# Optimization experiments

Hardware: AMD Instinct MI355X
Metric: run time of the kernel (lower is better)

## Reference

```python
import jax, jax.numpy as jnp
import numpy as np

N_KERNELS = 5
MUL_FACTOR = 2.0


def setup_inputs() -> dict:
    key = jax.random.key(0)
    k1, k2 = jax.random.split(key)
    x = jax.random.normal(k1, (8192, 64), dtype=jnp.float32)
    y = jax.random.normal(k2, (8192, 64), dtype=jnp.float32)
    return {"x": x, "y": y}


def reference(x, y):
    # bandwidth multipliers: mul_factor ** (arange(n) - n//2) -> [0.25,0.5,1,2,4]
    mults = MUL_FACTOR ** (jnp.arange(N_KERNELS, dtype=jnp.float32) - N_KERNELS // 2)

    z = jnp.concatenate([x, y], axis=0)  # [N, d], N = n + m
    n = x.shape[0]
    N = z.shape[0]

    # squared pairwise L2 distances: ||a||^2 + ||b||^2 - 2 a.b, clamped at 0
    sq = jnp.sum(z * z, axis=-1)  # [N]
    d2 = jnp.maximum(sq[:, None] + sq[None, :] - 2.0 * (z @ z.T), 0.0)  # [N, N]

    # data-dependent bandwidth: sum(d2) / (N^2 - N)
    bw = jnp.sum(d2) / (N * N - N)

    # multi-bandwidth RBF kernel, summed over kernels: [N, N]
    K = jnp.sum(jnp.exp(-d2[None, :, :] / (bw * mults)[:, None, None]), axis=0)

    XX = jnp.mean(K[:n, :n])
    XY = jnp.mean(K[:n, n:])
    YY = jnp.mean(K[n:, n:])
    return XX - 2.0 * XY + YY
```

## Files before the change

kernel.cpp:

```cpp
#include <hip/hip_runtime.h>
#include <hip/hip_bf16.h>

#define D 64

typedef __attribute__((ext_vector_type(8))) _Float16 half8;
typedef __attribute__((ext_vector_type(4))) float floatx4;

__global__ __launch_bounds__(256) void k_pre(const float* __restrict__ x, const float* __restrict__ y,
                                             int nx, _Float16* __restrict__ zh,
                                             float* __restrict__ sq, double* __restrict__ Tpart,
                                             float* __restrict__ Spart) {
    int tid = threadIdx.x;
    int lane = tid & 63, wid = tid >> 6;
    int t = blockIdx.x * 256 + tid;
    size_t e = (size_t)t * 8;
    int row = (int)(e >> 6);
    const float* src = (row < nx) ? (x + e) : (y + (e - (size_t)nx * D));
    float4 v0 = ((const float4*)src)[0];
    float4 v1 = ((const float4*)src)[1];
    half8 h;
    h[0]=(_Float16)v0.x; h[1]=(_Float16)v0.y; h[2]=(_Float16)v0.z; h[3]=(_Float16)v0.w;
    h[4]=(_Float16)v1.x; h[5]=(_Float16)v1.y; h[6]=(_Float16)v1.z; h[7]=(_Float16)v1.w;
    *(half8*)(zh + e) = h;
    float p = v0.x*v0.x + v0.y*v0.y + v0.z*v0.z + v0.w*v0.w
            + v1.x*v1.x + v1.y*v1.y + v1.z*v1.z + v1.w*v1.w;
    float s = p;
    s += __shfl_xor(s, 1);
    s += __shfl_xor(s, 2);
    s += __shfl_xor(s, 4);
    if ((tid & 7) == 0) sq[row] = s;

    __shared__ float colbuf[32][64];
    int rib = tid >> 3, cg = tid & 7;
    *(float4*)&colbuf[rib][cg * 8]     = v0;
    *(float4*)&colbuf[rib][cg * 8 + 4] = v1;

    double dp = (double)p;
    dp += __shfl_xor(dp, 1);
    dp += __shfl_xor(dp, 2);
    dp += __shfl_xor(dp, 4);
    dp += __shfl_xor(dp, 8);
    dp += __shfl_xor(dp, 16);
    dp += __shfl_xor(dp, 32);
    __shared__ double redw[4];
    if (lane == 0) redw[wid] = dp;
    __syncthreads();
    if (tid == 0) Tpart[blockIdx.x] = (redw[0] + redw[1]) + (redw[2] + redw[3]);

    if (tid < 64) {
        float cs = 0.f;
#pragma unroll
        for (int r2 = 0; r2 < 32; ++r2) cs += colbuf[r2][tid];
        Spart[blockIdx.x * 64 + tid] = cs;
    }
}

__global__ __launch_bounds__(256) void k_bw(const double* __restrict__ Tpart, int ntp,
                                            const float* __restrict__ Spart, int nsp,
                                            int N, float* __restrict__ cq_p) {
    int t = threadIdx.x;
    double Tp = 0.0;
    for (int b = t; b < ntp; b += 256) Tp += Tpart[b];

    int q = t >> 6, col = t & 63;
    int bpq = nsp >> 2;
    const float* sp = Spart + (size_t)(q * bpq) * 64 + col;
    float c0 = 0.f, c1 = 0.f, c2 = 0.f, c3 = 0.f;
    for (int b = 0; b < bpq; b += 4) {
        c0 += sp[(b + 0) * 64];
        c1 += sp[(b + 1) * 64];
        c2 += sp[(b + 2) * 64];
        c3 += sp[(b + 3) * 64];
    }
    __shared__ float cred[256];
    cred[t] = (c0 + c1) + (c2 + c3);

    __shared__ double red[256];
    red[t] = Tp;
    __syncthreads();
    for (int off = 128; off > 0; off >>= 1) {
        if (t < off) red[t] += red[t + off];
        __syncthreads();
    }
    double T = red[0];
    __shared__ double red2[64];
    if (t < 64) {
        float Sk = cred[t] + cred[t + 64] + cred[t + 128] + cred[t + 192];
        red2[t] = (double)Sk * (double)Sk;
    }
    __syncthreads();
    if (t == 0) {
        double S2 = 0.0;
        for (int i = 0; i < 64; ++i) S2 += red2[i];
        double sumd2 = 2.0 * (double)N * T - 2.0 * S2;
        double bw = sumd2 / ((double)N * (double)N - (double)N);
        cq_p[0] = (float)(1.4426950408889634 / (4.0 * bw));
    }
}

__global__ __launch_bounds__(256, 4) void k_mmd(const _Float16* __restrict__ zh,
                                                const float* __restrict__ sq,
                                                const float* __restrict__ cq_p,
                                                int nb, double* __restrict__ partial) {
    int bid = (nb - 1) - (int)blockIdx.x;
    int g = (int)((sqrtf(1.0f + 2.0f * (float)bid) - 1.0f) * 0.5f);
    while (2 * (g + 1) * (g + 2) <= bid) ++g;
    while (2 * g * (g + 1) > bid) --g;
    int r = bid - 2 * g * (g + 1);
    int gp1 = g + 1;
    int rig = r / gp1;
    int jc  = r - rig * gp1;
    int ib  = 4 * g + rig;

    int jstart = jc * 512;
    int jend   = (ib + 1) * 128;
    if (jend > jstart + 512) jend = jstart + 512;
    int njt = (jend - jstart) >> 4;
    int diag_j = ib * 128;

    int lane = threadIdx.x & 63;
    int wid  = threadIdx.x >> 6;
    int i0 = ib * 128 + wid * 32;

    float cq  = cq_p[0];
    float c2q = 2.0f * cq;

    int lrow = lane & 15;
    int kb = (lane >> 4) * 8;

    const _Float16* ar0 = zh + (size_t)(i0 + lrow) * D + kb;
    half8 a00 = *(const half8*)(ar0);
    half8 a01 = *(const half8*)(ar0 + 32);
    half8 a10 = *(const half8*)(ar0 + 16 * D);
    half8 a11 = *(const half8*)(ar0 + 16 * D + 32);

    int irh = (lane >> 4) * 4;
    float nai0[4], nai1[4];
#pragma unroll
    for (int rr = 0; rr < 4; ++rr) {
        nai0[rr] = -sq[i0 + irh + rr] * cq;
        nai1[rr] = -sq[i0 + 16 + irh + rr] * cq;
    }

    const _Float16* bptr = zh + (size_t)(jstart + lrow) * D + kb;
    const float* sqjp = sq + jstart + lrow;

    float acc = 0.f;

    auto compute = [&](half8 b0, half8 b1, float sqj, float wf) {
        float nbj = -sqj * cq;
        floatx4 d0 = {0.f, 0.f, 0.f, 0.f};
        floatx4 d1 = {0.f, 0.f, 0.f, 0.f};
        d0 = __builtin_amdgcn_mfma_f32_16x16x32_f16(a00, b0, d0, 0, 0, 0);
        d0 = __builtin_amdgcn_mfma_f32_16x16x32_f16(a01, b1, d0, 0, 0, 0);
        d1 = __builtin_amdgcn_mfma_f32_16x16x32_f16(a10, b0, d1, 0, 0, 0);
        d1 = __builtin_amdgcn_mfma_f32_16x16x32_f16(a11, b1, d1, 0, 0, 0);
        float part = 0.f;
#pragma unroll
        for (int rr = 0; rr < 4; ++rr) {
            float u0 = fminf(fmaf(d0[rr], c2q, nai0[rr] + nbj), 0.f);
            float u1 = fminf(fmaf(d1[rr], c2q, nai1[rr] + nbj), 0.f);
            float q0 = __builtin_amdgcn_exp2f(u0);
            float q1 = __builtin_amdgcn_exp2f(u1);
            float m01 = q0 * q0,   m11 = q1 * q1;
            float m02 = m01 * m01, m12 = m11 * m11;
            float m03 = m02 * m02, m13 = m12 * m12;
            float s0 = (q0 + m01) + (m02 + m03);
            float s1 = (q1 + m11) + (m12 + m13);
            part += fmaf(m03, m03, s0) + fmaf(m13, m13, s1);
        }
        acc = fmaf(part, wf, acc);
    };

    half8 b0A = *(const half8*)(bptr);
    half8 b1A = *(const half8*)(bptr + 32);
    float sA  = sqjp[0];
    half8 b0B = *(const half8*)(bptr + 16 * D);
    half8 b1B = *(const half8*)(bptr + 16 * D + 32);
    float sB  = sqjp[16];

    const _Float16* bp2 = bptr + 32 * D;
    const float* sp2 = sqjp + 32;
    int jcur = jstart;

    for (int jt = 0; jt + 2 < njt; jt += 2) {
        half8 p0 = *(const half8*)(bp2);
        half8 p1 = *(const half8*)(bp2 + 32);
        float ps = sp2[0];
        float wA = (jcur >= diag_j) ? 1.0f : 2.0f;
        compute(b0A, b1A, sA, wA);
        b0A = p0; b1A = p1; sA = ps;

        p0 = *(const half8*)(bp2 + 16 * D);
        p1 = *(const half8*)(bp2 + 16 * D + 32);
        ps = sp2[16];
        float wB = (jcur + 16 >= diag_j) ? 1.0f : 2.0f;
        compute(b0B, b1B, sB, wB);
        b0B = p0; b1B = p1; sB = ps;

        bp2 += 32 * D;
        sp2 += 32;
        jcur += 32;
    }
    {
        float wA = (jcur >= diag_j) ? 1.0f : 2.0f;
        compute(b0A, b1A, sA, wA);
        float wB = (jcur + 16 >= diag_j) ? 1.0f : 2.0f;
        compute(b0B, b1B, sB, wB);
    }

    double wacc = (double)acc;
    wacc += __shfl_xor(wacc, 1);
    wacc += __shfl_xor(wacc, 2);
    wacc += __shfl_xor(wacc, 4);
    wacc += __shfl_xor(wacc, 8);
    wacc += __shfl_xor(wacc, 16);
    wacc += __shfl_xor(wacc, 32);
    __shared__ double redw[4];
    if (lane == 0) redw[wid] = wacc;
    __syncthreads();
    if (threadIdx.x == 0) partial[bid] = (redw[0] + redw[1]) + (redw[2] + redw[3]);
}

__global__ __launch_bounds__(256) void k_final(const double* __restrict__ partial, int nb,
                                               int nxTile, int nxChunk,
                                               int nx, int ny, float* __restrict__ out) {
    int t = threadIdx.x;
    double sXX = 0.0, sXY = 0.0, sYY = 0.0;
    for (int p = t; p < nb; p += 256) {
        int g = (int)((sqrtf(1.0f + 2.0f * (float)p) - 1.0f) * 0.5f);
        while (2 * (g + 1) * (g + 2) <= p) ++g;
        while (2 * g * (g + 1) > p) --g;
        int r = p - 2 * g * (g + 1);
        int gp1 = g + 1;
        int rig = r / gp1;
        int jc  = r - rig * gp1;
        int ib  = 4 * g + rig;
        double v = partial[p];
        bool iX = ib < nxTile;
        bool jX = jc < nxChunk;
        if (iX && jX) sXX += v;
        else if (iX != jX) sXY += v;
        else sYY += v;
    }
    __shared__ double r0[256], r1[256], r2[256];
    r0[t] = sXX; r1[t] = sXY; r2[t] = sYY;
    __syncthreads();
    for (int off = 128; off > 0; off >>= 1) {
        if (t < off) {
            r0[t] += r0[t + off];
            r1[t] += r1[t + off];
            r2[t] += r2[t + off];
        }
        __syncthreads();
    }
    if (t == 0) {
        double XX = r0[0] / ((double)nx * (double)nx);
        double XY = r1[0] / (2.0 * (double)nx * (double)ny);
        double YY = r2[0] / ((double)ny * (double)ny);
        out[0] = (float)(XX - 2.0 * XY + YY);
    }
}

extern "C" void kernel_launch(void* const* d_in, const int* in_sizes, int n_in,
                              void* d_out, int out_size, void* d_ws, size_t ws_size,
                              hipStream_t stream) {
    const float* x = (const float*)d_in[0];
    const float* y = (const float*)d_in[1];
    float* out = (float*)d_out;

    int nx = in_sizes[0] / D;
    int ny = in_sizes[1] / D;
    int N  = nx + ny;

    int pre_blocks = (N * D / 8) / 256;
    int nT = N / 128;
    int ngr = nT / 4;
    int nb = 2 * ngr * (ngr + 1);
    int nxTile = nx / 128;
    int nxChunk = nx / 512;

    char* w = (char*)d_ws;
    double* Tpart   = (double*)(w + 0);
    double* partial = (double*)(w + 4096);
    float*  Spart   = (float*) (w + 20992);
    float*  sq      = (float*) (w + 152064);
    float*  cq      = (float*) (w + 217600);
    _Float16* zh    = (_Float16*)(w + 217664);

    k_pre   <<<pre_blocks, 256, 0, stream>>>(x, y, nx, zh, sq, Tpart, Spart);
    k_bw    <<<1, 256, 0, stream>>>(Tpart, pre_blocks, Spart, pre_blocks, N, cq);
    k_mmd   <<<nb, 256, 0, stream>>>(zh, sq, cq, nb, partial);
    k_final <<<1, 256, 0, stream>>>(partial, nb, nxTile, nxChunk, nx, ny, out);
}
```

Baseline: 148.7 us.

## Stage shared B tiles into swizzled LDS with async double buffering

Each wave used to load its own copy of the B-row tiles from global memory into registers. Now the block loads each 32-row B tile once into LDS using the direct global-to-LDS builtin, with an XOR swizzle to avoid bank conflicts, and double-buffers the tiles across iterations with a barrier per tile. All four waves then read B fragments from LDS. Launch bounds are also raised to target more resident blocks. The aim is to cut redundant global/L2 traffic, at the cost of a block-wide barrier per tile and possible register pressure at higher occupancy in an exp-heavy, mostly compute-bound loop.

```diff
diff --git a/kernel.cpp b/kernel.cpp
--- a/kernel.cpp
+++ b/kernel.cpp
@@ -5,6 +5,9 @@
 
 typedef __attribute__((ext_vector_type(8))) _Float16 half8;
 typedef __attribute__((ext_vector_type(4))) float floatx4;
+
+typedef __attribute__((address_space(1))) unsigned int gu32_t;
+typedef __attribute__((address_space(3))) unsigned int lu32_t;
 
 __global__ __launch_bounds__(256) void k_pre(const float* __restrict__ x, const float* __restrict__ y,
                                              int nx, _Float16* __restrict__ zh,
@@ -98,7 +101,7 @@
     }
 }
 
-__global__ __launch_bounds__(256, 4) void k_mmd(const _Float16* __restrict__ zh,
+__global__ __launch_bounds__(256, 6) void k_mmd(const _Float16* __restrict__ zh,
                                                 const float* __restrict__ sq,
                                                 const float* __restrict__ cq_p,
                                                 int nb, double* __restrict__ partial) {
@@ -115,18 +118,20 @@
     int jstart = jc * 512;
     int jend   = (ib + 1) * 128;
     if (jend > jstart + 512) jend = jstart + 512;
-    int njt = (jend - jstart) >> 4;
+    int nt = (jend - jstart) >> 5;
     int diag_j = ib * 128;
 
-    int lane = threadIdx.x & 63;
-    int wid  = threadIdx.x >> 6;
+    int tid  = threadIdx.x;
+    int lane = tid & 63;
+    int wid  = tid >> 6;
     int i0 = ib * 128 + wid * 32;
 
     float cq  = cq_p[0];
     float c2q = 2.0f * cq;
 
     int lrow = lane & 15;
-    int kb = (lane >> 4) * 8;
+    int c2   = lane >> 4;
+    int kb   = c2 * 8;
 
     const _Float16* ar0 = zh + (size_t)(i0 + lrow) * D + kb;
     half8 a00 = *(const half8*)(ar0);
@@ -134,7 +139,7 @@
     half8 a10 = *(const half8*)(ar0 + 16 * D);
     half8 a11 = *(const half8*)(ar0 + 16 * D + 32);
 
-    int irh = (lane >> 4) * 4;
+    int irh = c2 * 4;
     float nai0[4], nai1[4];
 #pragma unroll
     for (int rr = 0; rr < 4; ++rr) {
@@ -142,71 +147,63 @@
         nai1[rr] = -sq[i0 + 16 + irh + rr] * cq;
     }
 
-    const _Float16* bptr = zh + (size_t)(jstart + lrow) * D + kb;
-    const float* sqjp = sq + jstart + lrow;
+    __shared__ __align__(16) _Float16 bsm[2][32 * 64];
+    int srow = tid >> 3;
+    int scc  = tid & 7;
+    int sc   = scc ^ (srow & 7);
+    const char* zbase = (const char*)zh + (size_t)jstart * 128 + srow * 128 + sc * 16;
+    char* ldsw = (char*)&bsm[0][0] + wid * 1024;
+
+    auto STAGE = [&](int buf, int tile) {
+        const char* src = zbase + (size_t)tile * (32 * 128);
+        __builtin_amdgcn_global_load_lds((const gu32_t*)(const void*)src,
+                                         (lu32_t*)(void*)(ldsw + buf * 4096),
+                                         16, 0, 0);
+    };
 
     float acc = 0.f;
 
-    auto compute = [&](half8 b0, half8 b1, float sqj, float wf) {
-        float nbj = -sqj * cq;
-        floatx4 d0 = {0.f, 0.f, 0.f, 0.f};
-        floatx4 d1 = {0.f, 0.f, 0.f, 0.f};
-        d0 = __builtin_amdgcn_mfma_f32_16x16x32_f16(a00, b0, d0, 0, 0, 0);
-        d0 = __builtin_amdgcn_mfma_f32_16x16x32_f16(a01, b1, d0, 0, 0, 0);
-        d1 = __builtin_amdgcn_mfma_f32_16x16x32_f16(a10, b0, d1, 0, 0, 0);
-        d1 = __builtin_amdgcn_mfma_f32_16x16x32_f16(a11, b1, d1, 0, 0, 0);
-        float part = 0.f;
-#pragma unroll
-        for (int rr = 0; rr < 4; ++rr) {
-            float u0 = fminf(fmaf(d0[rr], c2q, nai0[rr] + nbj), 0.f);
-            float u1 = fminf(fmaf(d1[rr], c2q, nai1[rr] + nbj), 0.f);
-            float q0 = __builtin_amdgcn_exp2f(u0);
-            float q1 = __builtin_amdgcn_exp2f(u1);
-            float m01 = q0 * q0,   m11 = q1 * q1;
-            float m02 = m01 * m01, m12 = m11 * m11;
-            float m03 = m02 * m02, m13 = m12 * m12;
-            float s0 = (q0 + m01) + (m02 + m03);
-            float s1 = (q1 + m11) + (m12 + m13);
-            part += fmaf(m03, m03, s0) + fmaf(m13, m13, s1);
+    STAGE(0, 0);
+    __syncthreads();
+
+    for (int t = 0; t < nt; ++t) {
+        if (t + 1 < nt) STAGE((t + 1) & 1, t + 1);
+        const char* bb = (const char*)&bsm[t & 1][0];
+        int j0t = jstart + t * 32;
+#pragma unroll
+        for (int s = 0; s < 2; ++s) {
+            int jr = s * 16 + lrow;
+            int swz = jr & 7;
+            half8 b0 = *(const half8*)(bb + jr * 128 + ((c2 ^ swz) * 16));
+            half8 b1 = *(const half8*)(bb + jr * 128 + (((c2 + 4) ^ swz) * 16));
+            float sqj = sq[j0t + s * 16 + lrow];
+
+            floatx4 d0 = {0.f, 0.f, 0.f, 0.f};
+            floatx4 d1 = {0.f, 0.f, 0.f, 0.f};
+            d0 = __builtin_amdgcn_mfma_f32_16x16x32_f16(a00, b0, d0, 0, 0, 0);
+            d0 = __builtin_amdgcn_mfma_f32_16x16x32_f16(a01, b1, d0, 0, 0, 0);
+            d1 = __builtin_amdgcn_mfma_f32_16x16x32_f16(a10, b0, d1, 0, 0, 0);
+            d1 = __builtin_amdgcn_mfma_f32_16x16x32_f16(a11, b1, d1, 0, 0, 0);
+
+            float nbj = -sqj * cq;
+            float part = 0.f;
+#pragma unroll
+            for (int rr = 0; rr < 4; ++rr) {
+                float u0 = fminf(fmaf(d0[rr], c2q, nai0[rr] + nbj), 0.f);
+                float u1 = fminf(fmaf(d1[rr], c2q, nai1[rr] + nbj), 0.f);
+                float q0 = __builtin_amdgcn_exp2f(u0);
+                float q1 = __builtin_amdgcn_exp2f(u1);
+                float m01 = q0 * q0,   m11 = q1 * q1;
+                float m02 = m01 * m01, m12 = m11 * m11;
+                float m03 = m02 * m02, m13 = m12 * m12;
+                float s0 = (q0 + m01) + (m02 + m03);
+                float s1 = (q1 + m11) + (m12 + m13);
+                part += fmaf(m03, m03, s0) + fmaf(m13, m13, s1);
+            }
+            float wf = ((j0t + s * 16) >= diag_j) ? 1.0f : 2.0f;
+            acc = fmaf(part, wf, acc);
         }
-        acc = fmaf(part, wf, acc);
-    };
-
-    half8 b0A = *(const half8*)(bptr);
-    half8 b1A = *(const half8*)(bptr + 32);
-    float sA  = sqjp[0];
-    half8 b0B = *(const half8*)(bptr + 16 * D);
-    half8 b1B = *(const half8*)(bptr + 16 * D + 32);
-    float sB  = sqjp[16];
-
-    const _Float16* bp2 = bptr + 32 * D;
-    const float* sp2 = sqjp + 32;
-    int jcur = jstart;
-
-    for (int jt = 0; jt + 2 < njt; jt += 2) {
-        half8 p0 = *(const half8*)(bp2);
-        half8 p1 = *(const half8*)(bp2 + 32);
-        float ps = sp2[0];
-        float wA = (jcur >= diag_j) ? 1.0f : 2.0f;
-        compute(b0A, b1A, sA, wA);
-        b0A = p0; b1A = p1; sA = ps;
-
-        p0 = *(const half8*)(bp2 + 16 * D);
-        p1 = *(const half8*)(bp2 + 16 * D + 32);
-        ps = sp2[16];
-        float wB = (jcur + 16 >= diag_j) ? 1.0f : 2.0f;
-        compute(b0B, b1B, sB, wB);
-        b0B = p0; b1B = p1; sB = ps;
-
-        bp2 += 32 * D;
-        sp2 += 32;
-        jcur += 32;
-    }
-    {
-        float wA = (jcur >= diag_j) ? 1.0f : 2.0f;
-        compute(b0A, b1A, sA, wA);
-        float wB = (jcur + 16 >= diag_j) ? 1.0f : 2.0f;
-        compute(b0B, b1B, sB, wB);
+        __syncthreads();
     }
 
     double wacc = (double)acc;
@@ -216,10 +213,10 @@
     wacc += __shfl_xor(wacc, 8);
     wacc += __shfl_xor(wacc, 16);
     wacc += __shfl_xor(wacc, 32);
-    __shared__ double redw[4];
-    if (lane == 0) redw[wid] = wacc;
-    __syncthreads();
-    if (threadIdx.x == 0) partial[bid] = (redw[0] + redw[1]) + (redw[2] + redw[3]);
+    __shared__ double redr[4];
+    if (lane == 0) redr[wid] = wacc;
+    __syncthreads();
+    if (tid == 0) partial[bid] = (redr[0] + redr[1]) + (redr[2] + redr[3]);
 }
 
 __global__ __launch_bounds__(256) void k_final(const double* __restrict__ partial, int nb,
```

Result: faster. 129.0 us (-13.2%).
